# Kernel optimization log

Hardware: AMD Instinct MI355X
Metric: run time of the kernel (lower is better)

## Reference

```python
import jax, jax.numpy as jnp
import numpy as np
import math

DIM = 1024
WINDOW = 16
NUM_HEADS = 16
HEAD_DIM = DIM // NUM_HEADS
SCALE = math.sqrt(HEAD_DIM)
LN_EPS = 1e-5


def _gather_window(z, W):
    # z: [B, T, H, C] -> [B, T, H, W, C]; nb[:, t, :, w, :] = z[:, t-1-w] (zeros if t-1-w < 0)
    B, T, H, C = z.shape
    t = jnp.arange(T)[:, None]
    w = jnp.arange(W)[None, :]
    idx = t - 1 - w                      # [T, W]
    valid = idx >= 0
    idxc = jnp.clip(idx, 0, T - 1)
    nb = z[:, idxc]                      # [B, T, W, H, C]
    nb = jnp.where(valid[None, :, :, None, None], nb, jnp.zeros((), z.dtype))
    return nb.transpose(0, 1, 3, 2, 4)   # [B, T, H, W, C]


def setup_inputs() -> dict:
    key = jax.random.key(0)
    k0, k1, k2, k3 = jax.random.split(key, 4)
    B, T, D = 2, 4096, DIM
    x = jax.random.normal(k0, (B, T, D), dtype=jnp.float32)
    wq = jax.random.normal(k1, (D, D), dtype=jnp.float32) * 0.02
    wkv = jax.random.normal(k2, (2 * D, D), dtype=jnp.float32) * 0.02  # torch Linear weight layout [out,in]
    wo = jax.random.normal(k3, (D, D), dtype=jnp.float32) * 0.02
    gamma = jnp.ones((D,), dtype=jnp.float32)
    beta = jnp.zeros((D,), dtype=jnp.float32)
    return {"x": x, "wq": wq, "wkv": wkv, "wo": wo, "gamma": gamma, "beta": beta}


def reference(x, wq, wkv, wo, gamma, beta):
    B, T, D = x.shape
    H, HD, W = NUM_HEADS, HEAD_DIM, WINDOW
    q = (x @ wq.T).reshape(B, T, H, HD)
    kv = (x @ wkv.T).reshape(B, T, H, 2 * HD)
    nb_kv = _gather_window(kv, W)                    # [B, T, H, W, 2*HD]
    nb_k, nb_v = nb_kv[..., :HD], nb_kv[..., HD:]
    tau = jax.nn.sigmoid(jnp.einsum('bthd,bthwd->bthw', q, nb_k) / SCALE)
    msg = jnp.einsum('bthw,bthwd->bthd', tau, nb_v)  # [B, T, H, HD]
    y = x + msg.reshape(B, T, D) @ wo.T
    mu = jnp.mean(y, axis=-1, keepdims=True)
    var = jnp.mean((y - mu) ** 2, axis=-1, keepdims=True)
    out = (y - mu) * jax.lax.rsqrt(var + LN_EPS) * gamma + beta
    return out
```

## Files before the change

### kernel.cpp

```cpp
#include <hip/hip_runtime.h>
#include <hip/hip_bf16.h>

#define D_MODEL 1024
#define SEQ_T   4096
#define NBATCH  2
#define NHEADS  16
#define HEAD_D  64
#define WIN     16

typedef __attribute__((ext_vector_type(8))) short bf16x8;
typedef __attribute__((ext_vector_type(8))) unsigned short u16x8;
typedef __attribute__((ext_vector_type(4))) float f32x4;

__device__ __forceinline__ unsigned short f2bf(float f) {
  union { float f; unsigned int u; } v; v.f = f;
  unsigned int r = v.u + 0x7fffu + ((v.u >> 16) & 1u);
  return (unsigned short)(r >> 16);
}
__device__ __forceinline__ float bf2f(unsigned short u) {
  union { unsigned int u; float f; } v; v.u = ((unsigned int)u) << 16;
  return v.f;
}

__global__ __launch_bounds__(256) void cast_f32_bf16(const float4* __restrict__ src,
                                                     ushort* __restrict__ dst, int n4) {
  int i = blockIdx.x * 256 + threadIdx.x;
  if (i >= n4) return;
  float4 v = src[i];
  ushort4 o;
  o.x = f2bf(v.x); o.y = f2bf(v.y); o.z = f2bf(v.z); o.w = f2bf(v.w);
  *(ushort4*)(dst + (size_t)i * 4) = o;
}

__global__ __launch_bounds__(256) void cast_weights(const float4* __restrict__ wq,
                                                    const float4* __restrict__ wkv,
                                                    const float4* __restrict__ wo,
                                                    ushort* __restrict__ dst) {
  int i = blockIdx.x * 256 + threadIdx.x;
  const float4* src;
  int off;
  if (i < 262144) { src = wq; off = 0; }
  else if (i < 786432) { src = wkv; off = 262144; }
  else { src = wo; off = 786432; }
  float4 v = src[i - off];
  ushort4 o;
  o.x = f2bf(v.x); o.y = f2bf(v.y); o.z = f2bf(v.z); o.w = f2bf(v.w);
  *(ushort4*)(dst + (size_t)i * 4) = o;
}

#define SBAR() __builtin_amdgcn_s_barrier()
#define FENCE() __builtin_amdgcn_sched_barrier(0)
#define LGKM0() asm volatile("s_waitcnt lgkmcnt(0)" ::: "memory")
#define VMC6() asm volatile("s_waitcnt vmcnt(6)" ::: "memory")

template <int EPI>
__global__ __launch_bounds__(512, 2) void gemm_2ph(const ushort* __restrict__ A,
                                                   const ushort* __restrict__ Bt,
                                                   ushort* __restrict__ Cb,
                                                   float* __restrict__ Cf,
                                                   const float* __restrict__ resid,
                                                   int M, int N, int K) {
  extern __shared__ char smem[];
  const int NTK = K >> 6;
  const int tid = threadIdx.x;
  const int wid = tid >> 6;
  const int lane = tid & 63;
  const int m0 = blockIdx.y * 256;
  const int n0 = blockIdx.x * 128;

  const int l8 = lane >> 3;
  const int lchunk = (lane & 7) ^ (l8 & 7);
  const ushort* pA = A + (size_t)(m0 + wid * 16 + l8) * K + lchunk * 8;
  const ushort* pB = Bt + (size_t)(n0 + wid * 16 + l8) * K + lchunk * 8;

#define STAGE_A(h, kt, db)                                                                 \
  {                                                                                        \
    _Pragma("unroll") for (int j = 0; j < 2; ++j) {                                        \
      const ushort* gp = pA + (size_t)((h) * 128 + j * 8) * K + (size_t)(kt) * 64;         \
      char* lp = smem + (db) * 32768 + (h) * 16384 + (wid * 2 + j) * 1024;                 \
      __builtin_amdgcn_global_load_lds((const __attribute__((address_space(1))) void*)gp,  \
                                       (__attribute__((address_space(3))) void*)lp, 16, 0, 0); \
    }                                                                                      \
  }
#define STAGE_B(kt, db)                                                                    \
  {                                                                                        \
    _Pragma("unroll") for (int j = 0; j < 2; ++j) {                                        \
      const ushort* gp = pB + (size_t)(j * 8) * K + (size_t)(kt) * 64;                     \
      char* lp = smem + 65536 + (db) * 16384 + (wid * 2 + j) * 1024;                       \
      __builtin_amdgcn_global_load_lds((const __attribute__((address_space(1))) void*)gp,  \
                                       (__attribute__((address_space(3))) void*)lp, 16, 0, 0); \
    }                                                                                      \
  }

  const int fr = lane & 15;
  const int g = lane >> 4;
  const int wr = wid >> 2;
  const int wc = wid & 3;
  int aRow[4], bRow[2], ch[2];
#pragma unroll
  for (int mi = 0; mi < 4; ++mi) aRow[mi] = (wr * 64 + mi * 16 + fr) * 128;
#pragma unroll
  for (int ni = 0; ni < 2; ++ni) bRow[ni] = (wc * 32 + ni * 16 + fr) * 128;
#pragma unroll
  for (int kk = 0; kk < 2; ++kk) ch[kk] = ((kk * 4 + g) ^ (fr & 7)) * 16;

  f32x4 acc[2][4][2];
#pragma unroll
  for (int mq = 0; mq < 2; ++mq)
#pragma unroll
    for (int mi = 0; mi < 4; ++mi)
#pragma unroll
      for (int ni = 0; ni < 2; ++ni) acc[mq][mi][ni] = (f32x4){0.f, 0.f, 0.f, 0.f};

  bf16x8 a[4][2], bf[2][2];

  STAGE_A(0, 0, 0); STAGE_B(0, 0); STAGE_A(1, 0, 0);
  STAGE_A(0, 1, 1); STAGE_B(1, 1);
  VMC6();
  FENCE(); SBAR();

#define PHASE_MFMA(mq)                                                         \
  __builtin_amdgcn_s_setprio(1);                                               \
  _Pragma("unroll") for (int kk = 0; kk < 2; ++kk)                             \
    _Pragma("unroll") for (int mi = 0; mi < 4; ++mi)                           \
      _Pragma("unroll") for (int ni = 0; ni < 2; ++ni)                         \
        acc[mq][mi][ni] = __builtin_amdgcn_mfma_f32_16x16x32_bf16(             \
            a[mi][kk], bf[ni][kk], acc[mq][mi][ni], 0, 0, 0);                  \
  __builtin_amdgcn_s_setprio(0);

#pragma unroll 1
  for (int t = 0; t < NTK; ++t) {
    const int db = t & 1;
    const int u1 = (t + 1 < NTK) ? t + 1 : NTK - 1;
    const int u2 = (t + 2 < NTK) ? t + 2 : NTK - 1;
    const int d1 = u1 & 1, d2 = u2 & 1;
    const char* Ab = smem + db * 32768;
    const char* Bb = smem + 65536 + db * 16384;

#pragma unroll
    for (int mi = 0; mi < 4; ++mi)
#pragma unroll
      for (int kk = 0; kk < 2; ++kk)
        a[mi][kk] = *(const bf16x8*)(Ab + 0 * 16384 + aRow[mi] + ch[kk]);
#pragma unroll
    for (int ni = 0; ni < 2; ++ni)
#pragma unroll
      for (int kk = 0; kk < 2; ++kk)
        bf[ni][kk] = *(const bf16x8*)(Bb + bRow[ni] + ch[kk]);
    STAGE_A(1, u1, d1);
    FENCE(); SBAR(); LGKM0(); FENCE();
    PHASE_MFMA(0);
    FENCE(); VMC6(); SBAR();

#pragma unroll
    for (int mi = 0; mi < 4; ++mi)
#pragma unroll
      for (int kk = 0; kk < 2; ++kk)
        a[mi][kk] = *(const bf16x8*)(Ab + 1 * 16384 + aRow[mi] + ch[kk]);
    STAGE_A(0, u2, d2);
    STAGE_B(u2, d2);
    FENCE(); SBAR(); LGKM0(); FENCE();
    PHASE_MFMA(1);
    FENCE(); VMC6(); SBAR();
  }

  const int cc = lane & 15;
  const int cr4 = (lane >> 4) * 4;
#pragma unroll
  for (int mq = 0; mq < 2; ++mq)
#pragma unroll
    for (int mi = 0; mi < 4; ++mi)
#pragma unroll
      for (int ni = 0; ni < 2; ++ni)
#pragma unroll
        for (int r = 0; r < 4; ++r) {
          int row = m0 + mq * 128 + wr * 64 + mi * 16 + cr4 + r;
          int col = n0 + wc * 32 + ni * 16 + cc;
          size_t idx = (size_t)row * N + col;
          float v = acc[mq][mi][ni][r];
          if (EPI == 0) {
            Cb[idx] = f2bf(v);
          } else {
            Cf[idx] = v + resid[idx];
          }
        }
#undef STAGE_A
#undef STAGE_B
#undef PHASE_MFMA
}

__global__ __launch_bounds__(256) void attn_win_mfma(const ushort* __restrict__ qkv,
                                                     ushort* __restrict__ msg) {
  __shared__ ushort Ks[80][72];
  __shared__ ushort Vt[64][88];
  __shared__ ushort Ps[4][16][40];

  const int tile = blockIdx.x;
  const int h = blockIdx.y;
  const int b = blockIdx.z;
  const int t0 = tile * 64;
  const size_t rowbase = (size_t)b * SEQ_T;
  const int tid = threadIdx.x;
  const int wave = tid >> 6;
  const int lane = tid & 63;

  for (int chunk = tid; chunk < 1280; chunk += 256) {
    int r = chunk >> 4;
    int c = (chunk & 15) * 8;
    int t = t0 - 16 + r;
    u16x8 u = {0, 0, 0, 0, 0, 0, 0, 0};
    if (t >= 0)
      u = *(const u16x8*)(qkv + (rowbase + t) * 3072 + 1024 + (size_t)h * 128 + c);
    if (c < 64) {
      *(u16x8*)&Ks[r][c] = u;
    } else {
      int d0 = c - 64;
#pragma unroll
      for (int j = 0; j < 8; ++j) Vt[d0 + j][r] = u[j];
    }
  }
  __syncthreads();

  const int fr = lane & 15;
  const int g = lane >> 4;
  const int rbase = wave * 16;

  bf16x8 qa[2];
#pragma unroll
  for (int kk = 0; kk < 2; ++kk)
    qa[kk] = *(const bf16x8*)(qkv + (rowbase + t0 + wave * 16 + fr) * 3072 +
                              (size_t)h * 64 + kk * 32 + g * 8);

  f32x4 sacc[2];
  sacc[0] = (f32x4){0.f, 0.f, 0.f, 0.f};
  sacc[1] = (f32x4){0.f, 0.f, 0.f, 0.f};
#pragma unroll
  for (int kk = 0; kk < 2; ++kk) {
#pragma unroll
    for (int nt = 0; nt < 2; ++nt) {
      bf16x8 kb = *(const bf16x8*)&Ks[rbase + nt * 16 + fr][kk * 32 + g * 8];
      sacc[nt] = __builtin_amdgcn_mfma_f32_16x16x32_bf16(qa[kk], kb, sacc[nt], 0, 0, 0);
    }
  }

#pragma unroll
  for (int nt = 0; nt < 2; ++nt) {
    int tk = t0 - 16 + rbase + nt * 16 + fr;
#pragma unroll
    for (int reg = 0; reg < 4; ++reg) {
      int t = t0 + wave * 16 + g * 4 + reg;
      float tau = 0.f;
      if (tk >= 0 && tk >= t - WIN && tk <= t - 1)
        tau = 1.f / (1.f + __expf(-sacc[nt][reg] * 0.125f));
      Ps[wave][g * 4 + reg][nt * 16 + fr] = f2bf(tau);
    }
  }
  __syncthreads();

  bf16x8 pa = *(const bf16x8*)&Ps[wave][fr][g * 8];
#pragma unroll
  for (int ct = 0; ct < 4; ++ct) {
    bf16x8 vb = *(const bf16x8*)&Vt[ct * 16 + fr][rbase + g * 8];
    f32x4 m = __builtin_amdgcn_mfma_f32_16x16x32_bf16(pa, vb, (f32x4){0.f, 0.f, 0.f, 0.f}, 0, 0, 0);
#pragma unroll
    for (int reg = 0; reg < 4; ++reg) {
      int t = t0 + wave * 16 + g * 4 + reg;
      msg[(rowbase + t) * 1024 + (size_t)h * 64 + ct * 16 + fr] = f2bf(m[reg]);
    }
  }
}

__global__ __launch_bounds__(256) void layernorm_inplace(float* __restrict__ y,
                                                         const float* __restrict__ gamma,
                                                         const float* __restrict__ beta) {
  const int row = blockIdx.x;
  float* p = y + (size_t)row * D_MODEL;
  const int tid = threadIdx.x;
  float4 v = *(const float4*)&p[tid * 4];
  float s = v.x + v.y + v.z + v.w;
  float s2 = v.x * v.x + v.y * v.y + v.z * v.z + v.w * v.w;
#pragma unroll
  for (int m = 1; m < 64; m <<= 1) {
    s += __shfl_xor(s, m);
    s2 += __shfl_xor(s2, m);
  }
  __shared__ float red[8];
  const int wave = tid >> 6, lane = tid & 63;
  if (lane == 0) { red[wave] = s; red[4 + wave] = s2; }
  __syncthreads();
  s = red[0] + red[1] + red[2] + red[3];
  s2 = red[4] + red[5] + red[6] + red[7];
  const float mu = s * (1.f / D_MODEL);
  const float var = s2 * (1.f / D_MODEL) - mu * mu;
  const float rstd = rsqrtf(var + 1e-5f);
  float4 g = *(const float4*)&gamma[tid * 4];
  float4 be = *(const float4*)&beta[tid * 4];
  float4 o;
  o.x = (v.x - mu) * rstd * g.x + be.x;
  o.y = (v.y - mu) * rstd * g.y + be.y;
  o.z = (v.z - mu) * rstd * g.z + be.z;
  o.w = (v.w - mu) * rstd * g.w + be.w;
  *(float4*)&p[tid * 4] = o;
}

extern "C" void kernel_launch(void* const* d_in, const int* in_sizes, int n_in,
                              void* d_out, int out_size, void* d_ws, size_t ws_size,
                              hipStream_t stream) {
  (void)in_sizes; (void)n_in; (void)out_size; (void)ws_size;
  const float* x = (const float*)d_in[0];
  const float* wq = (const float*)d_in[1];
  const float* wkv = (const float*)d_in[2];
  const float* wo = (const float*)d_in[3];
  const float* gamma = (const float*)d_in[4];
  const float* beta = (const float*)d_in[5];
  float* out = (float*)d_out;

  ushort* xb = (ushort*)d_ws;
  ushort* wb = xb + (size_t)8192 * 1024;
  ushort* qkvb = wb + (size_t)4096 * 1024;
  ushort* msgb = qkvb + (size_t)8192 * 3072;

  const int M = NBATCH * SEQ_T;

  (void)hipFuncSetAttribute(reinterpret_cast<const void*>(&gemm_2ph<0>),
                            hipFuncAttributeMaxDynamicSharedMemorySize, 98304);
  (void)hipFuncSetAttribute(reinterpret_cast<const void*>(&gemm_2ph<1>),
                            hipFuncAttributeMaxDynamicSharedMemorySize, 98304);

  cast_f32_bf16<<<(M * D_MODEL / 4 + 255) / 256, 256, 0, stream>>>((const float4*)x, xb, M * D_MODEL / 4);
  cast_weights<<<4096, 256, 0, stream>>>((const float4*)wq, (const float4*)wkv,
                                         (const float4*)wo, wb);

  gemm_2ph<0><<<dim3(3072 / 128, M / 256), 512, 98304, stream>>>(xb, wb, qkvb, nullptr, nullptr,
                                                                 M, 3072, 1024);

  attn_win_mfma<<<dim3(SEQ_T / 64, NHEADS, NBATCH), 256, 0, stream>>>(qkvb, msgb);

  gemm_2ph<1><<<dim3(1024 / 128, M / 256), 512, 98304, stream>>>(msgb, wb + (size_t)3072 * 1024,
                                                                 nullptr, out, x, M, 1024, 1024);

  layernorm_inplace<<<M, 256, 0, stream>>>(out, gamma, beta);
}
```

Before: 140.4 us.

## Restructure GEMM warp tiling to split phases over N and simplify prefetch

Changes the 8-wave GEMM from two M-halves per tile to a 4x2 wave grid where each wave covers 64x64, with the two MFMA phases now splitting across N (B fragments) instead of M. The staging pipeline is rewritten: the whole A tile is loaded per k-step with B prefetched one step ahead and A two steps ahead, and the wait counts are adjusted. Scheduling fences are removed, so the compiler may reorder more freely. The aim is fewer LDS reads of A per phase and a simpler load/compute overlap, at the risk of less precise scheduling control and possible hazards in the double-buffer timing.

```diff
diff --git a/kernel.cpp b/kernel.cpp
--- a/kernel.cpp
+++ b/kernel.cpp
@@ -49,17 +49,16 @@
 }
 
 #define SBAR() __builtin_amdgcn_s_barrier()
-#define FENCE() __builtin_amdgcn_sched_barrier(0)
 #define LGKM0() asm volatile("s_waitcnt lgkmcnt(0)" ::: "memory")
-#define VMC6() asm volatile("s_waitcnt vmcnt(6)" ::: "memory")
+#define VMC(n) asm volatile("s_waitcnt vmcnt(" #n ")" ::: "memory")
 
 template <int EPI>
-__global__ __launch_bounds__(512, 2) void gemm_2ph(const ushort* __restrict__ A,
-                                                   const ushort* __restrict__ Bt,
-                                                   ushort* __restrict__ Cb,
-                                                   float* __restrict__ Cf,
-                                                   const float* __restrict__ resid,
-                                                   int M, int N, int K) {
+__global__ __launch_bounds__(512, 2) void gemm_8w(const ushort* __restrict__ A,
+                                                  const ushort* __restrict__ Bt,
+                                                  ushort* __restrict__ Cb,
+                                                  float* __restrict__ Cf,
+                                                  const float* __restrict__ resid,
+                                                  int M, int N, int K) {
   extern __shared__ char smem[];
   const int NTK = K >> 6;
   const int tid = threadIdx.x;
@@ -70,14 +69,14 @@
 
   const int l8 = lane >> 3;
   const int lchunk = (lane & 7) ^ (l8 & 7);
-  const ushort* pA = A + (size_t)(m0 + wid * 16 + l8) * K + lchunk * 8;
-  const ushort* pB = Bt + (size_t)(n0 + wid * 16 + l8) * K + lchunk * 8;
-
-#define STAGE_A(h, kt, db)                                                                 \
+  const ushort* pA = A + (size_t)(m0 + wid * 8 + l8) * K + lchunk * 8;
+  const ushort* pB = Bt + (size_t)(n0 + wid * 8 + l8) * K + lchunk * 8;
+
+#define STAGE_A(kt, db)                                                                    \
   {                                                                                        \
-    _Pragma("unroll") for (int j = 0; j < 2; ++j) {                                        \
-      const ushort* gp = pA + (size_t)((h) * 128 + j * 8) * K + (size_t)(kt) * 64;         \
-      char* lp = smem + (db) * 32768 + (h) * 16384 + (wid * 2 + j) * 1024;                 \
+    _Pragma("unroll") for (int j = 0; j < 4; ++j) {                                        \
+      const ushort* gp = pA + (size_t)(j * 64) * K + (size_t)(kt) * 64;                    \
+      char* lp = smem + (db) * 32768 + (j * 8 + wid) * 1024;                               \
       __builtin_amdgcn_global_load_lds((const __attribute__((address_space(1))) void*)gp,  \
                                        (__attribute__((address_space(3))) void*)lp, 16, 0, 0); \
     }                                                                                      \
@@ -85,8 +84,8 @@
 #define STAGE_B(kt, db)                                                                    \
   {                                                                                        \
     _Pragma("unroll") for (int j = 0; j < 2; ++j) {                                        \
-      const ushort* gp = pB + (size_t)(j * 8) * K + (size_t)(kt) * 64;                     \
-      char* lp = smem + 65536 + (db) * 16384 + (wid * 2 + j) * 1024;                       \
+      const ushort* gp = pB + (size_t)(j * 64) * K + (size_t)(kt) * 64;                    \
+      char* lp = smem + 65536 + (db) * 16384 + (j * 8 + wid) * 1024;                       \
       __builtin_amdgcn_global_load_lds((const __attribute__((address_space(1))) void*)gp,  \
                                        (__attribute__((address_space(3))) void*)lp, 16, 0, 0); \
     }                                                                                      \
@@ -94,38 +93,39 @@
 
   const int fr = lane & 15;
   const int g = lane >> 4;
-  const int wr = wid >> 2;
-  const int wc = wid & 3;
-  int aRow[4], bRow[2], ch[2];
+  const int wr = wid >> 1;
+  const int wc = wid & 1;
+  int aRow[4], bRow[2][2], ch[2];
 #pragma unroll
   for (int mi = 0; mi < 4; ++mi) aRow[mi] = (wr * 64 + mi * 16 + fr) * 128;
 #pragma unroll
-  for (int ni = 0; ni < 2; ++ni) bRow[ni] = (wc * 32 + ni * 16 + fr) * 128;
+  for (int nq = 0; nq < 2; ++nq)
+#pragma unroll
+    for (int ni = 0; ni < 2; ++ni) bRow[nq][ni] = (wc * 64 + nq * 32 + ni * 16 + fr) * 128;
 #pragma unroll
   for (int kk = 0; kk < 2; ++kk) ch[kk] = ((kk * 4 + g) ^ (fr & 7)) * 16;
 
   f32x4 acc[2][4][2];
 #pragma unroll
-  for (int mq = 0; mq < 2; ++mq)
+  for (int nq = 0; nq < 2; ++nq)
 #pragma unroll
     for (int mi = 0; mi < 4; ++mi)
 #pragma unroll
-      for (int ni = 0; ni < 2; ++ni) acc[mq][mi][ni] = (f32x4){0.f, 0.f, 0.f, 0.f};
-
-  bf16x8 a[4][2], bf[2][2];
-
-  STAGE_A(0, 0, 0); STAGE_B(0, 0); STAGE_A(1, 0, 0);
-  STAGE_A(0, 1, 1); STAGE_B(1, 1);
-  VMC6();
-  FENCE(); SBAR();
-
-#define PHASE_MFMA(mq)                                                         \
+      for (int ni = 0; ni < 2; ++ni) acc[nq][mi][ni] = (f32x4){0.f, 0.f, 0.f, 0.f};
+
+  bf16x8 a[4][2], b0[2][2], b1[2][2];
+
+  STAGE_A(0, 0); STAGE_B(0, 0); STAGE_A(1, 1);
+  VMC(4);
+  SBAR();
+
+#define PHASE_MFMA(nq, bfr)                                                    \
   __builtin_amdgcn_s_setprio(1);                                               \
   _Pragma("unroll") for (int kk = 0; kk < 2; ++kk)                             \
     _Pragma("unroll") for (int mi = 0; mi < 4; ++mi)                           \
       _Pragma("unroll") for (int ni = 0; ni < 2; ++ni)                         \
-        acc[mq][mi][ni] = __builtin_amdgcn_mfma_f32_16x16x32_bf16(             \
-            a[mi][kk], bf[ni][kk], acc[mq][mi][ni], 0, 0, 0);                  \
+        acc[nq][mi][ni] = __builtin_amdgcn_mfma_f32_16x16x32_bf16(             \
+            a[mi][kk], bfr[ni][kk], acc[nq][mi][ni], 0, 0, 0);                 \
   __builtin_amdgcn_s_setprio(0);
 
 #pragma unroll 1
@@ -141,43 +141,44 @@
     for (int mi = 0; mi < 4; ++mi)
 #pragma unroll
       for (int kk = 0; kk < 2; ++kk)
-        a[mi][kk] = *(const bf16x8*)(Ab + 0 * 16384 + aRow[mi] + ch[kk]);
+        a[mi][kk] = *(const bf16x8*)(Ab + aRow[mi] + ch[kk]);
 #pragma unroll
     for (int ni = 0; ni < 2; ++ni)
 #pragma unroll
       for (int kk = 0; kk < 2; ++kk)
-        bf[ni][kk] = *(const bf16x8*)(Bb + bRow[ni] + ch[kk]);
-    STAGE_A(1, u1, d1);
-    FENCE(); SBAR(); LGKM0(); FENCE();
-    PHASE_MFMA(0);
-    FENCE(); VMC6(); SBAR();
-
-#pragma unroll
-    for (int mi = 0; mi < 4; ++mi)
+        b0[ni][kk] = *(const bf16x8*)(Bb + bRow[0][ni] + ch[kk]);
+    STAGE_B(u1, d1);
+    LGKM0();
+    PHASE_MFMA(0, b0);
+    VMC(2);
+    SBAR();
+
+#pragma unroll
+    for (int ni = 0; ni < 2; ++ni)
 #pragma unroll
       for (int kk = 0; kk < 2; ++kk)
-        a[mi][kk] = *(const bf16x8*)(Ab + 1 * 16384 + aRow[mi] + ch[kk]);
-    STAGE_A(0, u2, d2);
-    STAGE_B(u2, d2);
-    FENCE(); SBAR(); LGKM0(); FENCE();
-    PHASE_MFMA(1);
-    FENCE(); VMC6(); SBAR();
+        b1[ni][kk] = *(const bf16x8*)(Bb + bRow[1][ni] + ch[kk]);
+    STAGE_A(u2, d2);
+    LGKM0();
+    PHASE_MFMA(1, b1);
+    VMC(4);
+    SBAR();
   }
 
   const int cc = lane & 15;
   const int cr4 = (lane >> 4) * 4;
 #pragma unroll
-  for (int mq = 0; mq < 2; ++mq)
+  for (int nq = 0; nq < 2; ++nq)
 #pragma unroll
     for (int mi = 0; mi < 4; ++mi)
 #pragma unroll
       for (int ni = 0; ni < 2; ++ni)
 #pragma unroll
         for (int r = 0; r < 4; ++r) {
-          int row = m0 + mq * 128 + wr * 64 + mi * 16 + cr4 + r;
-          int col = n0 + wc * 32 + ni * 16 + cc;
+          int row = m0 + wr * 64 + mi * 16 + cr4 + r;
+          int col = n0 + wc * 64 + nq * 32 + ni * 16 + cc;
           size_t idx = (size_t)row * N + col;
-          float v = acc[mq][mi][ni][r];
+          float v = acc[nq][mi][ni][r];
           if (EPI == 0) {
             Cb[idx] = f2bf(v);
           } else {
@@ -322,22 +323,22 @@
 
   const int M = NBATCH * SEQ_T;
 
-  (void)hipFuncSetAttribute(reinterpret_cast<const void*>(&gemm_2ph<0>),
+  (void)hipFuncSetAttribute(reinterpret_cast<const void*>(&gemm_8w<0>),
                             hipFuncAttributeMaxDynamicSharedMemorySize, 98304);
-  (void)hipFuncSetAttribute(reinterpret_cast<const void*>(&gemm_2ph<1>),
+  (void)hipFuncSetAttribute(reinterpret_cast<const void*>(&gemm_8w<1>),
                             hipFuncAttributeMaxDynamicSharedMemorySize, 98304);
 
   cast_f32_bf16<<<(M * D_MODEL / 4 + 255) / 256, 256, 0, stream>>>((const float4*)x, xb, M * D_MODEL / 4);
   cast_weights<<<4096, 256, 0, stream>>>((const float4*)wq, (const float4*)wkv,
                                          (const float4*)wo, wb);
 
-  gemm_2ph<0><<<dim3(3072 / 128, M / 256), 512, 98304, stream>>>(xb, wb, qkvb, nullptr, nullptr,
-                                                                 M, 3072, 1024);
+  gemm_8w<0><<<dim3(3072 / 128, M / 256), 512, 98304, stream>>>(xb, wb, qkvb, nullptr, nullptr,
+                                                                M, 3072, 1024);
 
   attn_win_mfma<<<dim3(SEQ_T / 64, NHEADS, NBATCH), 256, 0, stream>>>(qkvb, msgb);
 
-  gemm_2ph<1><<<dim3(1024 / 128, M / 256), 512, 98304, stream>>>(msgb, wb + (size_t)3072 * 1024,
-                                                                 nullptr, out, x, M, 1024, 1024);
+  gemm_8w<1><<<dim3(1024 / 128, M / 256), 512, 98304, stream>>>(msgb, wb + (size_t)3072 * 1024,
+                                                                nullptr, out, x, M, 1024, 1024);
 
   layernorm_inplace<<<M, 256, 0, stream>>>(out, gamma, beta);
 }
```

Result: faster. 135.5 us (-3.5%).
